# Kernel tuning notes

Hardware: AMD Instinct MI355X
Metric: run time of the kernel (lower is better)

Reference implementation:

```python
import jax, jax.numpy as jnp
import numpy as np

N_CLASSES = 3

def setup_inputs() -> dict:
    key = jax.random.key(0)
    k1, k2 = jax.random.split(key)
    feats = jax.random.normal(k1, (16, 1024, 1024, 3), dtype=jnp.float32)
    inst = jax.random.randint(k2, (16, 1024, 1024, 1), 0, N_CLASSES, dtype=jnp.int32)
    return {"feats": feats, "inst": inst}

def reference(feats, inst):
    # Faithful to the TF layer: for each class c, compute the GLOBAL mean of
    # feats over all masked elements (mask tiled across the 3 channels, over
    # the whole batch), then scatter that scalar back into masked positions.
    # Class masks are disjoint, so the sequential update order is benign.
    for c in range(N_CLASSES):
        mask = (inst == c)                                   # [B,H,W,1]
        maskb = jnp.broadcast_to(mask, feats.shape)          # [B,H,W,3]
        cnt = jnp.sum(maskb.astype(feats.dtype))             # scalar count (incl. channels)
        feats_mean = jnp.sum(jnp.where(maskb, feats, 0)) / cnt
        feats = jnp.where(maskb, feats_mean, feats)
    return feats
```

## Files before the change

kernel.cpp:

```cpp
#include <hip/hip_runtime.h>


#define RBLK 2048

typedef float vfloat4 __attribute__((ext_vector_type(4)));
typedef int vint4 __attribute__((ext_vector_type(4)));

__device__ inline double wred_d(double v) {
#pragma unroll
    for (int off = 32; off; off >>= 1) v += __shfl_down(v, off, 64);
    return v;
}
__device__ inline unsigned wred_u(unsigned v) {
#pragma unroll
    for (int off = 32; off; off >>= 1) v += __shfl_down(v, off, 64);
    return v;
}

__device__ inline void acc_group(vint4 cls, vfloat4 a, vfloat4 b, vfloat4 c,
                                 double& s0, double& s1, double& s2,
                                 unsigned& c0, unsigned& c1, unsigned& c2) {
    double d0 = (double)(a.x + a.y + a.z);
    double d1 = (double)(a.w + b.x + b.y);
    double d2 = (double)(b.z + b.w + c.x);
    double d3 = (double)(c.y + c.z + c.w);
    s0 += (cls.x == 0) ? d0 : 0.0;
    s1 += (cls.x == 1) ? d0 : 0.0;
    s2 += (cls.x == 2) ? d0 : 0.0;
    s0 += (cls.y == 0) ? d1 : 0.0;
    s1 += (cls.y == 1) ? d1 : 0.0;
    s2 += (cls.y == 2) ? d1 : 0.0;
    s0 += (cls.z == 0) ? d2 : 0.0;
    s1 += (cls.z == 1) ? d2 : 0.0;
    s2 += (cls.z == 2) ? d2 : 0.0;
    s0 += (cls.w == 0) ? d3 : 0.0;
    s1 += (cls.w == 1) ? d3 : 0.0;
    s2 += (cls.w == 2) ? d3 : 0.0;
    c0 += (unsigned)(cls.x == 0) + (unsigned)(cls.y == 0) +
          (unsigned)(cls.z == 0) + (unsigned)(cls.w == 0);
    c1 += (unsigned)(cls.x == 1) + (unsigned)(cls.y == 1) +
          (unsigned)(cls.z == 1) + (unsigned)(cls.w == 1);
    c2 += (unsigned)(cls.x == 2) + (unsigned)(cls.y == 2) +
          (unsigned)(cls.z == 2) + (unsigned)(cls.w == 2);
}

__device__ inline unsigned pack4(vint4 cls) {
    return (unsigned)((cls.x & 3) | ((cls.y & 3) << 2) |
                      ((cls.z & 3) << 4) | ((cls.w & 3) << 6));
}

__global__ __launch_bounds__(256) void reduce_k(const float* __restrict__ feats,
                                                const int* __restrict__ inst,
                                                double* __restrict__ psum,
                                                unsigned* __restrict__ pcnt,
                                                unsigned short* __restrict__ codes2,
                                                int npix8) {
    int tid = blockIdx.x * 256 + threadIdx.x;
    int stride = gridDim.x * 256;
    double s0 = 0.0, s1 = 0.0, s2 = 0.0;
    unsigned c0 = 0, c1 = 0, c2 = 0;
    const vint4* inst4 = (const vint4*)inst;
    for (int i = tid; i < npix8; i += stride) {
        vint4 clsA = inst4[(size_t)i * 2 + 0];
        vint4 clsB = inst4[(size_t)i * 2 + 1];
        const vfloat4* f = (const vfloat4*)(feats + (size_t)i * 24);
        vfloat4 fa0 = f[0], fa1 = f[1], fa2 = f[2];
        vfloat4 fb0 = f[3], fb1 = f[4], fb2 = f[5];
        acc_group(clsA, fa0, fa1, fa2, s0, s1, s2, c0, c1, c2);
        acc_group(clsB, fb0, fb1, fb2, s0, s1, s2, c0, c1, c2);
        codes2[i] = (unsigned short)(pack4(clsA) | (pack4(clsB) << 8));
    }
    s0 = wred_d(s0); s1 = wred_d(s1); s2 = wred_d(s2);
    c0 = wred_u(c0); c1 = wred_u(c1); c2 = wred_u(c2);

    __shared__ double ls[4][3];
    __shared__ unsigned lc[4][3];
    int wid = threadIdx.x >> 6;
    int lane = threadIdx.x & 63;
    if (lane == 0) {
        ls[wid][0] = s0; ls[wid][1] = s1; ls[wid][2] = s2;
        lc[wid][0] = c0; lc[wid][1] = c1; lc[wid][2] = c2;
    }
    __syncthreads();
    if (threadIdx.x < 3) {
        int c = threadIdx.x;
        double s = ls[0][c] + ls[1][c] + ls[2][c] + ls[3][c];
        unsigned cc = lc[0][c] + lc[1][c] + lc[2][c] + lc[3][c];
        psum[blockIdx.x * 3 + c] = s;
        pcnt[blockIdx.x * 3 + c] = cc;
    }
}

__global__ __launch_bounds__(256) void scatter_k(const double* __restrict__ psum,
                                                 const unsigned* __restrict__ pcnt,
                                                 const unsigned short* __restrict__ codes2,
                                                 float* __restrict__ out,
                                                 int nblk, int npix8) {
    double s0 = 0.0, s1 = 0.0, s2 = 0.0;
    unsigned c0 = 0, c1 = 0, c2 = 0;
    for (int i = threadIdx.x; i < nblk; i += 256) {
        s0 += psum[i * 3 + 0]; s1 += psum[i * 3 + 1]; s2 += psum[i * 3 + 2];
        c0 += pcnt[i * 3 + 0]; c1 += pcnt[i * 3 + 1]; c2 += pcnt[i * 3 + 2];
    }
    s0 = wred_d(s0); s1 = wred_d(s1); s2 = wred_d(s2);
    c0 = wred_u(c0); c1 = wred_u(c1); c2 = wred_u(c2);

    __shared__ double ls[4][3];
    __shared__ unsigned lc[4][3];
    __shared__ float lmean[3];
    int wid = threadIdx.x >> 6;
    int lane = threadIdx.x & 63;
    if (lane == 0) {
        ls[wid][0] = s0; ls[wid][1] = s1; ls[wid][2] = s2;
        lc[wid][0] = c0; lc[wid][1] = c1; lc[wid][2] = c2;
    }
    __syncthreads();
    if (threadIdx.x < 3) {
        int c = threadIdx.x;
        double s = ls[0][c] + ls[1][c] + ls[2][c] + ls[3][c];
        unsigned cc = lc[0][c] + lc[1][c] + lc[2][c] + lc[3][c];
        lmean[c] = (float)(s / (3.0 * (double)cc));
    }
    __syncthreads();
    float m0 = lmean[0], m1 = lmean[1], m2 = lmean[2];

    int tid = blockIdx.x * 256 + threadIdx.x;
    int stride = gridDim.x * 256;
    for (int i = tid; i < npix8; i += stride) {
        unsigned cc8 = codes2[i];
        float v[8];
#pragma unroll
        for (int p = 0; p < 8; ++p) {
            unsigned k = (cc8 >> (2 * p)) & 3;
            v[p] = (k == 1) ? m1 : ((k == 2) ? m2 : m0);
        }
        vfloat4* o = (vfloat4*)(out + (size_t)i * 24);
        vfloat4 o0 = {v[0], v[0], v[0], v[1]};
        vfloat4 o1 = {v[1], v[1], v[2], v[2]};
        vfloat4 o2 = {v[2], v[3], v[3], v[3]};
        vfloat4 o3 = {v[4], v[4], v[4], v[5]};
        vfloat4 o4 = {v[5], v[5], v[6], v[6]};
        vfloat4 o5 = {v[6], v[7], v[7], v[7]};
        o[0] = o0; o[1] = o1; o[2] = o2; o[3] = o3; o[4] = o4; o[5] = o5;
    }
}

extern "C" void kernel_launch(void* const* d_in, const int* in_sizes, int n_in,
                              void* d_out, int out_size, void* d_ws, size_t ws_size,
                              hipStream_t stream) {
    const float* feats = (const float*)d_in[0];
    const int* inst = (const int*)d_in[1];
    float* out = (float*)d_out;

    int npix = in_sizes[1];
    int npix8 = npix >> 3;

    double* psum = (double*)d_ws;
    unsigned* pcnt = (unsigned*)(psum + RBLK * 3);
    unsigned short* codes2 = (unsigned short*)(pcnt + RBLK * 3);

    reduce_k<<<RBLK, 256, 0, stream>>>(feats, inst, psum, pcnt, codes2, npix8);
    scatter_k<<<RBLK, 256, 0, stream>>>(psum, pcnt, codes2, out, RBLK, npix8);
}
```

Before: 414.2 us.

## Fuse reduce and scatter into one cooperative kernel with register-held codes

Merges the reduction and scatter kernels into one cooperative launch that uses a grid-wide sync between the two phases. Each thread keeps its packed class codes in a small register array, so the codes buffer is no longer written to and read back from global memory, and one kernel launch is dropped. In exchange the grid is fixed at 1024 blocks with a per-thread iteration cap of 8 (MAXITER), which only holds for inputs whose size fits within 1024×256×8 groups of 8 pixels. It also pays for a grid barrier and lower occupancy per block.

```diff
diff --git a/kernel.cpp b/kernel.cpp
--- a/kernel.cpp
+++ b/kernel.cpp
@@ -1,7 +1,11 @@
 #include <hip/hip_runtime.h>
+#include <hip/hip_cooperative_groups.h>
+
+namespace cg = cooperative_groups;
 
 
-#define RBLK 2048
+#define NBLK 1024
+#define MAXITER 8
 
 typedef float vfloat4 __attribute__((ext_vector_type(4)));
 typedef int vint4 __attribute__((ext_vector_type(4)));
@@ -49,18 +53,22 @@
                       ((cls.z & 3) << 4) | ((cls.w & 3) << 6));
 }
 
-__global__ __launch_bounds__(256) void reduce_k(const float* __restrict__ feats,
-                                                const int* __restrict__ inst,
-                                                double* __restrict__ psum,
-                                                unsigned* __restrict__ pcnt,
-                                                unsigned short* __restrict__ codes2,
-                                                int npix8) {
-    int tid = blockIdx.x * 256 + threadIdx.x;
-    int stride = gridDim.x * 256;
+__global__ __launch_bounds__(256, 4) void fused_k(const float* __restrict__ feats,
+                                                  const int* __restrict__ inst,
+                                                  double* __restrict__ psum,
+                                                  unsigned* __restrict__ pcnt,
+                                                  float* __restrict__ out,
+                                                  int npix8) {
+    cg::grid_group grid = cg::this_grid();
+    const int tid = blockIdx.x * 256 + threadIdx.x;
+    const int stride = NBLK * 256;
+
     double s0 = 0.0, s1 = 0.0, s2 = 0.0;
     unsigned c0 = 0, c1 = 0, c2 = 0;
+    unsigned codes[MAXITER];
     const vint4* inst4 = (const vint4*)inst;
-    for (int i = tid; i < npix8; i += stride) {
+    int niter = 0;
+    for (int i = tid; i < npix8; i += stride, ++niter) {
         vint4 clsA = inst4[(size_t)i * 2 + 0];
         vint4 clsB = inst4[(size_t)i * 2 + 1];
         const vfloat4* f = (const vfloat4*)(feats + (size_t)i * 24);
@@ -68,15 +76,16 @@
         vfloat4 fb0 = f[3], fb1 = f[4], fb2 = f[5];
         acc_group(clsA, fa0, fa1, fa2, s0, s1, s2, c0, c1, c2);
         acc_group(clsB, fb0, fb1, fb2, s0, s1, s2, c0, c1, c2);
-        codes2[i] = (unsigned short)(pack4(clsA) | (pack4(clsB) << 8));
+        codes[niter] = pack4(clsA) | (pack4(clsB) << 8);
     }
     s0 = wred_d(s0); s1 = wred_d(s1); s2 = wred_d(s2);
     c0 = wred_u(c0); c1 = wred_u(c1); c2 = wred_u(c2);
 
     __shared__ double ls[4][3];
     __shared__ unsigned lc[4][3];
-    int wid = threadIdx.x >> 6;
-    int lane = threadIdx.x & 63;
+    __shared__ float lmean[3];
+    const int wid = threadIdx.x >> 6;
+    const int lane = threadIdx.x & 63;
     if (lane == 0) {
         ls[wid][0] = s0; ls[wid][1] = s1; ls[wid][2] = s2;
         lc[wid][0] = c0; lc[wid][1] = c1; lc[wid][2] = c2;
@@ -84,35 +93,24 @@
     __syncthreads();
     if (threadIdx.x < 3) {
         int c = threadIdx.x;
-        double s = ls[0][c] + ls[1][c] + ls[2][c] + ls[3][c];
-        unsigned cc = lc[0][c] + lc[1][c] + lc[2][c] + lc[3][c];
-        psum[blockIdx.x * 3 + c] = s;
-        pcnt[blockIdx.x * 3 + c] = cc;
+        psum[blockIdx.x * 3 + c] = ls[0][c] + ls[1][c] + ls[2][c] + ls[3][c];
+        pcnt[blockIdx.x * 3 + c] = lc[0][c] + lc[1][c] + lc[2][c] + lc[3][c];
     }
-}
 
-__global__ __launch_bounds__(256) void scatter_k(const double* __restrict__ psum,
-                                                 const unsigned* __restrict__ pcnt,
-                                                 const unsigned short* __restrict__ codes2,
-                                                 float* __restrict__ out,
-                                                 int nblk, int npix8) {
-    double s0 = 0.0, s1 = 0.0, s2 = 0.0;
-    unsigned c0 = 0, c1 = 0, c2 = 0;
-    for (int i = threadIdx.x; i < nblk; i += 256) {
-        s0 += psum[i * 3 + 0]; s1 += psum[i * 3 + 1]; s2 += psum[i * 3 + 2];
-        c0 += pcnt[i * 3 + 0]; c1 += pcnt[i * 3 + 1]; c2 += pcnt[i * 3 + 2];
+    grid.sync();
+
+    double t0 = 0.0, t1 = 0.0, t2 = 0.0;
+    unsigned u0 = 0, u1 = 0, u2 = 0;
+    for (int i = threadIdx.x; i < NBLK; i += 256) {
+        t0 += psum[i * 3 + 0]; t1 += psum[i * 3 + 1]; t2 += psum[i * 3 + 2];
+        u0 += pcnt[i * 3 + 0]; u1 += pcnt[i * 3 + 1]; u2 += pcnt[i * 3 + 2];
     }
-    s0 = wred_d(s0); s1 = wred_d(s1); s2 = wred_d(s2);
-    c0 = wred_u(c0); c1 = wred_u(c1); c2 = wred_u(c2);
-
-    __shared__ double ls[4][3];
-    __shared__ unsigned lc[4][3];
-    __shared__ float lmean[3];
-    int wid = threadIdx.x >> 6;
-    int lane = threadIdx.x & 63;
+    t0 = wred_d(t0); t1 = wred_d(t1); t2 = wred_d(t2);
+    u0 = wred_u(u0); u1 = wred_u(u1); u2 = wred_u(u2);
+    __syncthreads();
     if (lane == 0) {
-        ls[wid][0] = s0; ls[wid][1] = s1; ls[wid][2] = s2;
-        lc[wid][0] = c0; lc[wid][1] = c1; lc[wid][2] = c2;
+        ls[wid][0] = t0; ls[wid][1] = t1; ls[wid][2] = t2;
+        lc[wid][0] = u0; lc[wid][1] = u1; lc[wid][2] = u2;
     }
     __syncthreads();
     if (threadIdx.x < 3) {
@@ -122,12 +120,11 @@
         lmean[c] = (float)(s / (3.0 * (double)cc));
     }
     __syncthreads();
-    float m0 = lmean[0], m1 = lmean[1], m2 = lmean[2];
+    const float m0 = lmean[0], m1 = lmean[1], m2 = lmean[2];
 
-    int tid = blockIdx.x * 256 + threadIdx.x;
-    int stride = gridDim.x * 256;
-    for (int i = tid; i < npix8; i += stride) {
-        unsigned cc8 = codes2[i];
+    int j = 0;
+    for (int i = tid; i < npix8; i += stride, ++j) {
+        unsigned cc8 = codes[j];
         float v[8];
 #pragma unroll
         for (int p = 0; p < 8; ++p) {
@@ -156,9 +153,10 @@
     int npix8 = npix >> 3;
 
     double* psum = (double*)d_ws;
-    unsigned* pcnt = (unsigned*)(psum + RBLK * 3);
-    unsigned short* codes2 = (unsigned short*)(pcnt + RBLK * 3);
+    unsigned* pcnt = (unsigned*)(psum + NBLK * 3);
 
-    reduce_k<<<RBLK, 256, 0, stream>>>(feats, inst, psum, pcnt, codes2, npix8);
-    scatter_k<<<RBLK, 256, 0, stream>>>(psum, pcnt, codes2, out, RBLK, npix8);
+    void* args[] = {(void*)&feats, (void*)&inst, (void*)&psum,
+                    (void*)&pcnt, (void*)&out, (void*)&npix8};
+    hipLaunchCooperativeKernel((const void*)fused_k, dim3(NBLK), dim3(256),
+                               args, 0, stream);
 }
```

Measured after the change: 525.4 us. 1.27x slower.
